# Kernel optimization log

Measured on AMD Instinct MI355X. Metric: run time of the kernel, lower is better.

Reference implementation:

```python
import jax, jax.numpy as jnp
import numpy as np


def _sample_choices(prob_weights, key):
    # softmax over edge-type dim, take P(NORMAL_EDGE)=index 1
    prob_edge = jax.nn.softmax(prob_weights, axis=-1)[..., 1]  # [out, in]
    k_bern, k_fix = jax.random.split(key)
    choices = jax.random.bernoulli(k_bern, prob_edge).astype(prob_weights.dtype)  # [out, in]
    # zero-connection fixup: rows with no sampled edge get one random connection
    out_f, in_f = choices.shape
    conn_count = jnp.sum(choices, axis=-1)  # [out]
    rand_cols = jax.random.randint(k_fix, (out_f,), 0, in_f)  # [out]
    fix = ((conn_count == 0)[:, None] & (jnp.arange(in_f)[None, :] == rand_cols[:, None]))
    choices = choices + fix.astype(choices.dtype)
    # selected edges -> 0, unselected -> 1 (min operator branch; no *-1 negation)
    mask = jnp.abs(choices - 1.0)
    return mask


def reference(x, prob_weights):
    # x: [B, in], prob_weights: [out, in, 2]
    mask = _sample_choices(prob_weights, jax.random.key(42))  # [out, in]
    # result[b, o] = min_i (x[b, i] + mask[o, i])  -- [B, out, in] intermediate
    operator_inputs = x[:, None, :] + mask[None, :, :]
    return jnp.min(operator_inputs, axis=-1)  # [B, out]


def setup_inputs() -> dict:
    key = jax.random.key(0)
    k_x, k_w = jax.random.split(key)
    B, IN, OUT = 512, 512, 512
    x = jax.random.uniform(k_x, (B, IN), dtype=jnp.float32)
    prob_weights = jax.random.uniform(k_w, (OUT, IN, 2), dtype=jnp.float32)
    return {"x": x, "prob_weights": prob_weights}
```

## Files before the change

kernel.cpp:

```cpp
#include <hip/hip_runtime.h>
#include <cstdint>

__host__ __device__ inline void threefry2x32(uint32_t k0, uint32_t k1,
                                             uint32_t x0, uint32_t x1,
                                             uint32_t& o0, uint32_t& o1) {
  const uint32_t ks2 = k0 ^ k1 ^ 0x1BD11BDAu;
  uint32_t v0 = x0 + k0, v1 = x1 + k1;
#define RL(v, r) (((v) << (r)) | ((v) >> (32 - (r))))
#define RND4(a, b, c, d)                                                       \
  v0 += v1; v1 = RL(v1, a); v1 ^= v0;                                          \
  v0 += v1; v1 = RL(v1, b); v1 ^= v0;                                          \
  v0 += v1; v1 = RL(v1, c); v1 ^= v0;                                          \
  v0 += v1; v1 = RL(v1, d); v1 ^= v0;
  RND4(13, 15, 26, 6)  v0 += k1;  v1 += ks2 + 1u;
  RND4(17, 29, 16, 24) v0 += ks2; v1 += k0 + 2u;
  RND4(13, 15, 26, 6)  v0 += k0;  v1 += k1 + 3u;
  RND4(17, 29, 16, 24) v0 += k1;  v1 += ks2 + 4u;
  RND4(13, 15, 26, 6)  v0 += ks2; v1 += k0 + 5u;
#undef RND4
#undef RL
  o0 = v0; o1 = v1;
}

#define IN_F 512
#define OUT_F 512
#define BATCH 512

__global__ __launch_bounds__(512) void gen_mask_kernel(
    const float* __restrict__ pw, float* __restrict__ M,
    uint32_t kb0, uint32_t kb1, uint32_t kl0, uint32_t kl1) {
  const int o = blockIdx.x;
  const int i = threadIdx.x;

  const float2 w = ((const float2*)pw)[o * IN_F + i];
  const float mx = fmaxf(w.x, w.y);
  const float e0 = expf(w.x - mx);
  const float e1 = expf(w.y - mx);
  const float p = e1 / (e0 + e1);

  const uint32_t n = (uint32_t)(o * IN_F + i);
  uint32_t h0, h1;
  threefry2x32(kb0, kb1, 0u, n, h0, h1);
  const uint32_t bits = h0 ^ h1;
  const float u = __uint_as_float((bits >> 9) | 0x3F800000u) - 1.0f;
  const bool c = u < p;

  __shared__ unsigned long long words[8];
  __shared__ int cnt;
  if (i == 0) cnt = 0;
  __syncthreads();
  const unsigned long long bal = __ballot(c);
  if ((i & 63) == 0) {
    words[i >> 6] = bal;
    atomicAdd(&cnt, __popcll(bal));
  }
  __syncthreads();
  if (cnt == 0 && i == 0) {
    uint32_t c0, c1;
    threefry2x32(kl0, kl1, 0u, (uint32_t)o, c0, c1);
    const uint32_t rb = c0 ^ c1;
    const uint32_t col = rb & (IN_F - 1);
    words[col >> 6] |= (1ull << (col & 63u));
  }
  __syncthreads();
  const bool sel = (words[i >> 6] >> (i & 63)) & 1ull;
  M[o * IN_F + i] = sel ? 0.0f : 1e9f;
}

#define BT 32
#define OT 16
#define KT 128

__global__ __launch_bounds__(256) void minplus_kernel(
    const float* __restrict__ x, const float* __restrict__ M,
    float* __restrict__ out) {
  __shared__ float xs[KT][BT + 1];
  __shared__ float ms[KT][OT + 1];

  const int tid = threadIdx.x;
  const int tx = tid & 15;
  const int ty = tid >> 4;
  const int b0 = blockIdx.x * BT;
  const int o0 = blockIdx.y * OT;

  const int sr = tid >> 5;
  const int sc = (tid & 31) * 4;

  float acc0 = 1e30f, acc1 = 1e30f;

  for (int kt = 0; kt < IN_F; kt += KT) {
#pragma unroll
    for (int j = 0; j < 4; ++j) {
      const int r = j * 8 + sr;
      const float4 v = *(const float4*)&x[(b0 + r) * IN_F + kt + sc];
      xs[sc + 0][r] = v.x; xs[sc + 1][r] = v.y;
      xs[sc + 2][r] = v.z; xs[sc + 3][r] = v.w;
    }
#pragma unroll
    for (int j = 0; j < 2; ++j) {
      const int r = j * 8 + sr;
      const float4 v = *(const float4*)&M[(o0 + r) * IN_F + kt + sc];
      ms[sc + 0][r] = v.x; ms[sc + 1][r] = v.y;
      ms[sc + 2][r] = v.z; ms[sc + 3][r] = v.w;
    }
    __syncthreads();
#pragma unroll 16
    for (int k = 0; k < KT; ++k) {
      const float2 xv = *(const float2*)&xs[k][tx * 2];
      const float mv = ms[k][ty];
      acc0 = fminf(acc0, xv.x + mv);
      acc1 = fminf(acc1, xv.y + mv);
    }
    __syncthreads();
  }

  out[(b0 + tx * 2 + 0) * OUT_F + o0 + ty] = acc0;
  out[(b0 + tx * 2 + 1) * OUT_F + o0 + ty] = acc1;
}

extern "C" void kernel_launch(void* const* d_in, const int* in_sizes, int n_in,
                              void* d_out, int out_size, void* d_ws, size_t ws_size,
                              hipStream_t stream) {
  (void)in_sizes; (void)n_in; (void)out_size; (void)ws_size;
  const float* x = (const float*)d_in[0];
  const float* pw = (const float*)d_in[1];
  float* M = (float*)d_ws;
  float* out = (float*)d_out;

  uint32_t kb0, kb1, kf0, kf1, kl0, kl1;
  threefry2x32(0u, 42u, 0u, 0u, kb0, kb1);
  threefry2x32(0u, 42u, 0u, 1u, kf0, kf1);
  threefry2x32(kf0, kf1, 0u, 1u, kl0, kl1);

  gen_mask_kernel<<<dim3(OUT_F), dim3(IN_F), 0, stream>>>(pw, M, kb0, kb1, kl0, kl1);
  minplus_kernel<<<dim3(BATCH / BT, OUT_F / OT), dim3(256), 0, stream>>>(x, M, out);
}
```

Baseline: 75.31 us.

## Restructure min-plus kernel to register-held x rows with wave-uniform mask loads and split-K

The min-plus kernel no longer stages x and mask tiles through LDS. Each lane keeps one batch row's x slice in registers, and the mask rows are read with wave-uniform addresses, which the compiler can turn into scalar loads. The K dimension is split across 4 wave pairs, and the partial minima are reduced through shared memory at the end. This removes the per-tile LDS traffic and barriers, at the cost of more registers and a final cross-wave reduction, and it depends on the mask loads actually being scalarized.

```diff
diff --git a/kernel.cpp b/kernel.cpp
--- a/kernel.cpp
+++ b/kernel.cpp
@@ -67,55 +67,58 @@
   M[o * IN_F + i] = sel ? 0.0f : 1e9f;
 }
 
-#define BT 32
-#define OT 16
-#define KT 128
-
-__global__ __launch_bounds__(256) void minplus_kernel(
+__global__ __launch_bounds__(512) void minplus_kernel(
     const float* __restrict__ x, const float* __restrict__ M,
     float* __restrict__ out) {
-  __shared__ float xs[KT][BT + 1];
-  __shared__ float ms[KT][OT + 1];
+  const int tid = threadIdx.x;
+  const int lane = tid & 63;
+  const int wv = __builtin_amdgcn_readfirstlane(tid >> 6);
+  const int oh = wv & 1;
+  const int kq = wv >> 1;
+  const int b0 = blockIdx.x * 64;
+  const int o0 = blockIdx.y * 16;
+  const int kbase = kq * 128;
+  const float* xrow = x + (size_t)(b0 + lane) * IN_F + kbase;
 
-  const int tid = threadIdx.x;
-  const int tx = tid & 15;
-  const int ty = tid >> 4;
-  const int b0 = blockIdx.x * BT;
-  const int o0 = blockIdx.y * OT;
+  float acc[8];
+#pragma unroll
+  for (int i = 0; i < 8; ++i) acc[i] = 1e30f;
 
-  const int sr = tid >> 5;
-  const int sc = (tid & 31) * 4;
-
-  float acc0 = 1e30f, acc1 = 1e30f;
-
-  for (int kt = 0; kt < IN_F; kt += KT) {
+#pragma unroll 1
+  for (int ks = 0; ks < 4; ++ks) {
+    float xr[32];
 #pragma unroll
-    for (int j = 0; j < 4; ++j) {
-      const int r = j * 8 + sr;
-      const float4 v = *(const float4*)&x[(b0 + r) * IN_F + kt + sc];
-      xs[sc + 0][r] = v.x; xs[sc + 1][r] = v.y;
-      xs[sc + 2][r] = v.z; xs[sc + 3][r] = v.w;
+    for (int j = 0; j < 8; ++j) {
+      const float4 v = *(const float4*)(xrow + ks * 32 + j * 4);
+      xr[4 * j + 0] = v.x; xr[4 * j + 1] = v.y;
+      xr[4 * j + 2] = v.z; xr[4 * j + 3] = v.w;
     }
 #pragma unroll
-    for (int j = 0; j < 2; ++j) {
-      const int r = j * 8 + sr;
-      const float4 v = *(const float4*)&M[(o0 + r) * IN_F + kt + sc];
-      ms[sc + 0][r] = v.x; ms[sc + 1][r] = v.y;
-      ms[sc + 2][r] = v.z; ms[sc + 3][r] = v.w;
+    for (int oo = 0; oo < 8; ++oo) {
+      const float* mp = M + (size_t)(o0 + oh * 8 + oo) * IN_F + kbase + ks * 32;
+#pragma unroll
+      for (int j = 0; j < 32; ++j)
+        acc[oo] = fminf(acc[oo], xr[j] + mp[j]);
     }
-    __syncthreads();
-#pragma unroll 16
-    for (int k = 0; k < KT; ++k) {
-      const float2 xv = *(const float2*)&xs[k][tx * 2];
-      const float mv = ms[k][ty];
-      acc0 = fminf(acc0, xv.x + mv);
-      acc1 = fminf(acc1, xv.y + mv);
-    }
-    __syncthreads();
   }
 
-  out[(b0 + tx * 2 + 0) * OUT_F + o0 + ty] = acc0;
-  out[(b0 + tx * 2 + 1) * OUT_F + o0 + ty] = acc1;
+  __shared__ float part[8][8][65];
+#pragma unroll
+  for (int oo = 0; oo < 8; ++oo) part[wv][oo][lane] = acc[oo];
+  __syncthreads();
+
+  const int o_loc = tid & 15;
+  const int brow = tid >> 4;
+  const int oh2 = o_loc >> 3, oo2 = o_loc & 7;
+#pragma unroll
+  for (int ib = 0; ib < 2; ++ib) {
+    const int bl = brow + ib * 32;
+    float v = part[oh2][oo2][bl];
+    v = fminf(v, part[2 + oh2][oo2][bl]);
+    v = fminf(v, part[4 + oh2][oo2][bl]);
+    v = fminf(v, part[6 + oh2][oo2][bl]);
+    out[(size_t)(b0 + bl) * OUT_F + o0 + o_loc] = v;
+  }
 }
 
 extern "C" void kernel_launch(void* const* d_in, const int* in_sizes, int n_in,
@@ -133,5 +136,5 @@
   threefry2x32(kf0, kf1, 0u, 1u, kl0, kl1);
 
   gen_mask_kernel<<<dim3(OUT_F), dim3(IN_F), 0, stream>>>(pw, M, kb0, kb1, kl0, kl1);
-  minplus_kernel<<<dim3(BATCH / BT, OUT_F / OT), dim3(256), 0, stream>>>(x, M, out);
+  minplus_kernel<<<dim3(BATCH / 64, OUT_F / 16), dim3(512), 0, stream>>>(x, M, out);
 }
```

Result: slower. 81.36 us (+8.0%).

## Use 4x4 register tiles and split-K with a separate min-reduction kernel

Applied to the files above, without the earlier changes.

The min-plus kernel moves from a 2-output-per-thread 32x16 tile to a 4x4 register tile over a 64x64 block, so each shared-memory load feeds more operations. The K dimension is split four ways across blockIdx.z to keep the grid at 256 blocks, and each split writes a partial result to workspace. A new reduce kernel takes the elementwise min of the four partials. This adds an extra launch and about 4MB of partial writes and reads in exchange for better arithmetic intensity per LDS access.

```diff
diff --git a/kernel.cpp b/kernel.cpp
--- a/kernel.cpp
+++ b/kernel.cpp
@@ -67,55 +67,77 @@
   M[o * IN_F + i] = sel ? 0.0f : 1e9f;
 }
 
-#define BT 32
-#define OT 16
-#define KT 128
+#define BT 64
+#define OT 64
+#define KT 32
+#define NZ 4
+#define KZ (IN_F / NZ)
 
 __global__ __launch_bounds__(256) void minplus_kernel(
     const float* __restrict__ x, const float* __restrict__ M,
-    float* __restrict__ out) {
-  __shared__ float xs[KT][BT + 1];
-  __shared__ float ms[KT][OT + 1];
+    float* __restrict__ part) {
+  __shared__ float xs[KT][BT + 4];
+  __shared__ float ms[KT][OT + 4];
 
   const int tid = threadIdx.x;
   const int tx = tid & 15;
   const int ty = tid >> 4;
   const int b0 = blockIdx.x * BT;
   const int o0 = blockIdx.y * OT;
+  const int kb = blockIdx.z * KZ;
 
-  const int sr = tid >> 5;
-  const int sc = (tid & 31) * 4;
+  const int lr = tid >> 3;
+  const int lc = (tid & 7) * 4;
 
-  float acc0 = 1e30f, acc1 = 1e30f;
+  float4 acc[4];
+#pragma unroll
+  for (int i = 0; i < 4; ++i) acc[i] = make_float4(1e30f, 1e30f, 1e30f, 1e30f);
 
-  for (int kt = 0; kt < IN_F; kt += KT) {
-#pragma unroll
-    for (int j = 0; j < 4; ++j) {
-      const int r = j * 8 + sr;
-      const float4 v = *(const float4*)&x[(b0 + r) * IN_F + kt + sc];
-      xs[sc + 0][r] = v.x; xs[sc + 1][r] = v.y;
-      xs[sc + 2][r] = v.z; xs[sc + 3][r] = v.w;
-    }
+  for (int kt = 0; kt < KZ; kt += KT) {
 #pragma unroll
     for (int j = 0; j < 2; ++j) {
-      const int r = j * 8 + sr;
-      const float4 v = *(const float4*)&M[(o0 + r) * IN_F + kt + sc];
-      ms[sc + 0][r] = v.x; ms[sc + 1][r] = v.y;
-      ms[sc + 2][r] = v.z; ms[sc + 3][r] = v.w;
+      const int r = j * 32 + lr;
+      const float4 v = *(const float4*)&x[(b0 + r) * IN_F + kb + kt + lc];
+      xs[lc + 0][r] = v.x; xs[lc + 1][r] = v.y;
+      xs[lc + 2][r] = v.z; xs[lc + 3][r] = v.w;
+      const float4 w = *(const float4*)&M[(o0 + r) * IN_F + kb + kt + lc];
+      ms[lc + 0][r] = w.x; ms[lc + 1][r] = w.y;
+      ms[lc + 2][r] = w.z; ms[lc + 3][r] = w.w;
     }
     __syncthreads();
-#pragma unroll 16
+#pragma unroll 8
     for (int k = 0; k < KT; ++k) {
-      const float2 xv = *(const float2*)&xs[k][tx * 2];
-      const float mv = ms[k][ty];
-      acc0 = fminf(acc0, xv.x + mv);
-      acc1 = fminf(acc1, xv.y + mv);
+      const float4 xv = *(const float4*)&xs[k][tx * 4];
+      const float4 mv = *(const float4*)&ms[k][ty * 4];
+#pragma unroll
+      for (int i = 0; i < 4; ++i) {
+        const float xi = (i == 0) ? xv.x : (i == 1) ? xv.y : (i == 2) ? xv.z : xv.w;
+        acc[i].x = fminf(acc[i].x, xi + mv.x);
+        acc[i].y = fminf(acc[i].y, xi + mv.y);
+        acc[i].z = fminf(acc[i].z, xi + mv.z);
+        acc[i].w = fminf(acc[i].w, xi + mv.w);
+      }
     }
     __syncthreads();
   }
 
-  out[(b0 + tx * 2 + 0) * OUT_F + o0 + ty] = acc0;
-  out[(b0 + tx * 2 + 1) * OUT_F + o0 + ty] = acc1;
+  float* pz = part + (size_t)blockIdx.z * (BATCH * OUT_F);
+#pragma unroll
+  for (int i = 0; i < 4; ++i)
+    *(float4*)&pz[(size_t)(b0 + 4 * tx + i) * OUT_F + o0 + 4 * ty] = acc[i];
+}
+
+__global__ __launch_bounds__(256) void reduce_kernel(
+    const float* __restrict__ part, float* __restrict__ out) {
+  const int n = blockIdx.x * 256 + threadIdx.x;
+  float4 a = ((const float4*)part)[n];
+#pragma unroll
+  for (int z = 1; z < NZ; ++z) {
+    const float4 b = ((const float4*)(part + (size_t)z * BATCH * OUT_F))[n];
+    a.x = fminf(a.x, b.x); a.y = fminf(a.y, b.y);
+    a.z = fminf(a.z, b.z); a.w = fminf(a.w, b.w);
+  }
+  ((float4*)out)[n] = a;
 }
 
 extern "C" void kernel_launch(void* const* d_in, const int* in_sizes, int n_in,
@@ -125,6 +147,7 @@
   const float* x = (const float*)d_in[0];
   const float* pw = (const float*)d_in[1];
   float* M = (float*)d_ws;
+  float* part = (float*)d_ws + BATCH * OUT_F;
   float* out = (float*)d_out;
 
   uint32_t kb0, kb1, kf0, kf1, kl0, kl1;
@@ -133,5 +156,6 @@
   threefry2x32(kf0, kf1, 0u, 1u, kl0, kl1);
 
   gen_mask_kernel<<<dim3(OUT_F), dim3(IN_F), 0, stream>>>(pw, M, kb0, kb1, kl0, kl1);
-  minplus_kernel<<<dim3(BATCH / BT, OUT_F / OT), dim3(256), 0, stream>>>(x, M, out);
+  minplus_kernel<<<dim3(BATCH / BT, OUT_F / OT, NZ), dim3(256), 0, stream>>>(x, M, part);
+  reduce_kernel<<<dim3(BATCH * OUT_F / 4 / 256), dim3(256), 0, stream>>>(part, out);
 }
```

After: 77.26 us. +2.6%, slower.
